# Optimization experiments

Hardware: AMD Instinct MI355X
Metric: run time of the kernel (lower is better)

Reference implementation:

```python
import jax, jax.numpy as jnp
import numpy as np

EPS = 1e-8

def setup_inputs() -> dict:
    key = jax.random.key(0)
    k1, k2, k3, k4, k5 = jax.random.split(key, 5)
    B, S, d, H = 4, 1024, 512, 8
    hd = d // H
    x = jax.random.normal(k1, (B, S, d), dtype=jnp.float32)
    V = jax.random.normal(k2, (B, S, H, hd), dtype=jnp.float32)
    # binary biological mask [B, S, S]
    M = (jax.random.uniform(k3, (B, S, S)) > 0.5).astype(jnp.float32)
    in_proj_w = jax.random.normal(k4, (3 * d, d), dtype=jnp.float32) * 0.02
    in_proj_b = jnp.zeros((3 * d,), dtype=jnp.float32)
    out_w = jax.random.normal(k5, (d, d), dtype=jnp.float32) * 0.02
    out_b = jnp.zeros((d,), dtype=jnp.float32)
    return {"x": x, "V": V, "M": M, "in_proj_w": in_proj_w,
            "in_proj_b": in_proj_b, "out_w": out_w, "out_b": out_b}


def reference(x, V, M, in_proj_w, in_proj_b, out_w, out_b):
    B, S, d = x.shape
    H, hd = V.shape[2], V.shape[3]
    # packed QKV projection (torch MHA in_proj); V slice is computed by torch
    # but its result is discarded, so only Q,K slices influence the output.
    qkv = x @ in_proj_w.T + in_proj_b            # [B, S, 3d]
    q = qkv[..., :d].reshape(B, S, H, hd).transpose(0, 2, 1, 3)        # [B,H,S,hd]
    k = qkv[..., d:2 * d].reshape(B, S, H, hd).transpose(0, 2, 1, 3)   # [B,H,S,hd]
    scores = jnp.einsum("bhqd,bhkd->bhqk", q, k) / jnp.sqrt(jnp.float32(hd))
    A = jax.nn.softmax(scores, axis=-1)           # [B,H,S,S] per-head attn weights
    # biological mask + L1 renormalization (post-hoc, as in original)
    A_sparse = A * M[:, None, :, :]
    norm = jnp.sum(jnp.abs(A_sparse), axis=-1, keepdims=True) + EPS
    A_bar = A_sparse / norm
    # custom V: [B,S,H,hd] -> [B,H,S,hd]
    Vp = V.transpose(0, 2, 1, 3)
    out = jnp.einsum("bhqk,bhkd->bhqd", A_bar, Vp)  # [B,H,S,hd]
    out = out.transpose(0, 2, 1, 3).reshape(B, S, d)
    return out @ out_w.T + out_b
```

## Files before the change

### kernel.cpp

```cpp
#include <hip/hip_runtime.h>
#include <hip/hip_bf16.h>

#define BB 4
#define SS 1024
#define DD 512
#define HH 8
#define HD 64

typedef __attribute__((ext_vector_type(8))) short bf16x8;
typedef __attribute__((ext_vector_type(4))) float f32x4;

static __device__ __forceinline__ unsigned short f2b(float f) {
  union { float f; unsigned int u; } c; c.f = f;
  return (unsigned short)((c.u + 0x7fffu + ((c.u >> 16) & 1u)) >> 16);
}

__global__ __launch_bounds__(256) void prep(
    const float* __restrict__ x, const float* __restrict__ W1,
    const float* __restrict__ Wo, const float* __restrict__ Mmask,
    const float* __restrict__ V, unsigned short* __restrict__ xb,
    unsigned short* __restrict__ W1b, unsigned short* __restrict__ Wob,
    unsigned char* __restrict__ Mpack, unsigned short* __restrict__ Vt) {
  __shared__ float Ls[64][65];
  const int bid = blockIdx.x;
  const int tid = threadIdx.x;

  if (bid < 1408) {
    const float* src; unsigned short* dst; size_t off;
    if (bid < 1024) { src = x;  dst = xb;  off = ((size_t)bid * 256 + tid) * 8; }
    else if (bid < 1280) { src = W1; dst = W1b; off = ((size_t)(bid - 1024) * 256 + tid) * 8; }
    else { src = Wo; dst = Wob; off = ((size_t)(bid - 1280) * 256 + tid) * 8; }
    const float4 a = *(const float4*)(src + off);
    const float4 b = *(const float4*)(src + off + 4);
    union { unsigned short s[8]; uint4 v; } o;
    o.s[0] = f2b(a.x); o.s[1] = f2b(a.y); o.s[2] = f2b(a.z); o.s[3] = f2b(a.w);
    o.s[4] = f2b(b.x); o.s[5] = f2b(b.y); o.s[6] = f2b(b.z); o.s[7] = f2b(b.w);
    *(uint4*)(dst + off) = o.v;
  } else if (bid < 3456) {
    const size_t g = (size_t)(bid - 1408) * 256 + tid;
    const float4 a = *(const float4*)(Mmask + g * 8);
    const float4 b = *(const float4*)(Mmask + g * 8 + 4);
    unsigned v = 0;
    v |= (a.x > 0.5f) ? 1u : 0u;   v |= (a.y > 0.5f) ? 2u : 0u;
    v |= (a.z > 0.5f) ? 4u : 0u;   v |= (a.w > 0.5f) ? 8u : 0u;
    v |= (b.x > 0.5f) ? 16u : 0u;  v |= (b.y > 0.5f) ? 32u : 0u;
    v |= (b.z > 0.5f) ? 64u : 0u;  v |= (b.w > 0.5f) ? 128u : 0u;
    Mpack[g] = (unsigned char)v;
  } else {
    const int id = bid - 3456;
    const int s0 = (id & 15) * 64, h = (id >> 4) & 7, b = id >> 7;
    {
      const int r = tid >> 2, cs = (tid & 3) * 16;
      const float* src = V + ((size_t)((b * SS + s0 + r) * HH) + h) * HD + cs;
#pragma unroll
      for (int j = 0; j < 4; j++) {
        const float4 v = *(const float4*)(src + j * 4);
        Ls[r][cs + j * 4 + 0] = v.x; Ls[r][cs + j * 4 + 1] = v.y;
        Ls[r][cs + j * 4 + 2] = v.z; Ls[r][cs + j * 4 + 3] = v.w;
      }
    }
    __syncthreads();
    {
      const int d = tid >> 2, ss = (tid & 3) * 16;
      union { unsigned short s[16]; uint4 v[2]; } o;
#pragma unroll
      for (int j = 0; j < 16; j++) o.s[j] = f2b(Ls[ss + j][d]);
      unsigned short* dst =
          Vt + ((size_t)((b * HH + h) * HD + d)) * SS + s0 + ss;
      *(uint4*)dst = o.v[0];
      *(uint4*)(dst + 8) = o.v[1];
    }
  }
}

__global__ __launch_bounds__(256) void gemm_qk(
    const unsigned short* __restrict__ xb, const unsigned short* __restrict__ W1b,
    const float* __restrict__ bias, unsigned short* __restrict__ qkb) {
  __shared__ unsigned short As[128][40];
  __shared__ unsigned short Bs[64][40];
  const int tid = threadIdx.x;
  const int lane = tid & 63, wave = tid >> 6;
  const int l16 = lane & 15, quad = lane >> 4;
  const int row0 = blockIdx.y * 128, col0 = blockIdx.x * 64;

  f32x4 acc[2][4];
#pragma unroll
  for (int i = 0; i < 2; i++)
#pragma unroll
    for (int j = 0; j < 4; j++) acc[i][j] = (f32x4){0.f, 0.f, 0.f, 0.f};

  const int ra = tid >> 1, csa = (tid & 1) * 16;
  const int rb = tid >> 2, csb = (tid & 3) * 8;
  const unsigned short* ap = xb + (size_t)(row0 + ra) * DD + csa;
  const unsigned short* bp = W1b + (size_t)(col0 + rb) * DD + csb;

  uint4 pa0 = *(const uint4*)ap, pa1 = *(const uint4*)(ap + 8);
  uint4 pb = *(const uint4*)bp;

  for (int k0 = 0; k0 < DD; k0 += 32) {
    __syncthreads();
    *(uint4*)&As[ra][csa] = pa0;
    *(uint4*)&As[ra][csa + 8] = pa1;
    *(uint4*)&Bs[rb][csb] = pb;
    __syncthreads();
    if (k0 + 32 < DD) {
      pa0 = *(const uint4*)(ap + k0 + 32);
      pa1 = *(const uint4*)(ap + k0 + 40);
      pb = *(const uint4*)(bp + k0 + 32);
    }

    const bf16x8 a0 = *(const bf16x8*)&As[wave * 32 + l16][quad * 8];
    const bf16x8 a1 = *(const bf16x8*)&As[wave * 32 + 16 + l16][quad * 8];
#pragma unroll
    for (int nt = 0; nt < 4; nt++) {
      const bf16x8 bb = *(const bf16x8*)&Bs[nt * 16 + l16][quad * 8];
      acc[0][nt] = __builtin_amdgcn_mfma_f32_16x16x32_bf16(a0, bb, acc[0][nt], 0, 0, 0);
      acc[1][nt] = __builtin_amdgcn_mfma_f32_16x16x32_bf16(a1, bb, acc[1][nt], 0, 0, 0);
    }
  }

#pragma unroll
  for (int nt = 0; nt < 4; nt++) {
    const int col = col0 + nt * 16 + l16;
    const float bv = bias[col];
    const float scale = (col < DD) ? 0.125f : 1.0f;
#pragma unroll
    for (int mi = 0; mi < 2; mi++)
#pragma unroll
      for (int reg = 0; reg < 4; reg++) {
        const int row = row0 + wave * 32 + mi * 16 + quad * 4 + reg;
        qkb[(size_t)row * 1024 + col] = f2b((acc[mi][nt][reg] + bv) * scale);
      }
  }
}

__global__ __launch_bounds__(256) void gemm_out(
    const unsigned short* __restrict__ Ab, const unsigned short* __restrict__ Wob,
    const float* __restrict__ bias, float* __restrict__ out) {
  __shared__ unsigned short As[64][40];
  __shared__ unsigned short Bs[64][40];
  const int tid = threadIdx.x;
  const int lane = tid & 63, wave = tid >> 6;
  const int l16 = lane & 15, quad = lane >> 4;
  const int row0 = blockIdx.y * 64, col0 = blockIdx.x * 64;

  f32x4 acc[4];
#pragma unroll
  for (int j = 0; j < 4; j++) acc[j] = (f32x4){0.f, 0.f, 0.f, 0.f};

  const int r = tid >> 2, cs = (tid & 3) * 8;
  const unsigned short* ap = Ab + (size_t)(row0 + r) * DD + cs;
  const unsigned short* bp = Wob + (size_t)(col0 + r) * DD + cs;

  uint4 pa = *(const uint4*)ap;
  uint4 pb = *(const uint4*)bp;

  for (int k0 = 0; k0 < DD; k0 += 32) {
    __syncthreads();
    *(uint4*)&As[r][cs] = pa;
    *(uint4*)&Bs[r][cs] = pb;
    __syncthreads();
    if (k0 + 32 < DD) {
      pa = *(const uint4*)(ap + k0 + 32);
      pb = *(const uint4*)(bp + k0 + 32);
    }

    const bf16x8 a0 = *(const bf16x8*)&As[wave * 16 + l16][quad * 8];
#pragma unroll
    for (int nt = 0; nt < 4; nt++) {
      const bf16x8 bb = *(const bf16x8*)&Bs[nt * 16 + l16][quad * 8];
      acc[nt] = __builtin_amdgcn_mfma_f32_16x16x32_bf16(a0, bb, acc[nt], 0, 0, 0);
    }
  }

#pragma unroll
  for (int nt = 0; nt < 4; nt++) {
    const int col = col0 + nt * 16 + l16;
    const float bv = bias[col];
#pragma unroll
    for (int reg = 0; reg < 4; reg++) {
      const int row = row0 + wave * 16 + quad * 4 + reg;
      out[(size_t)row * DD + col] = acc[nt][reg] + bv;
    }
  }
}

__global__ __launch_bounds__(256) void flash_attn(
    const unsigned short* __restrict__ qkb, const unsigned short* __restrict__ Vt,
    const unsigned char* __restrict__ Mpack, unsigned short* __restrict__ attnb) {
  __shared__ unsigned short QP[64][72];
  __shared__ unsigned short Ks[64][72];
  __shared__ unsigned short Vs[64][72];
  __shared__ float SmT[4][16];

  const int tid = threadIdx.x;
  const int lane = tid & 63, wave = tid >> 6;
  const int l16 = lane & 15, quad = lane >> 4;
  const int q0 = blockIdx.x * 64;
  const int h = blockIdx.y;
  const int b = blockIdx.z;

  const int r = tid >> 2, cs = (tid & 3) * 16;

  {
    const unsigned short* s = qkb + (size_t)(b * SS + q0 + r) * 1024 + h * HD + cs;
    *(uint4*)&QP[r][cs] = *(const uint4*)s;
    *(uint4*)&QP[r][cs + 8] = *(const uint4*)(s + 8);
  }
  __syncthreads();
  const bf16x8 bQ0 = *(const bf16x8*)&QP[wave * 16 + l16][quad * 8];
  const bf16x8 bQ1 = *(const bf16x8*)&QP[wave * 16 + l16][32 + quad * 8];
  unsigned short(*Ps)[72] = (unsigned short(*)[72]) & QP[wave * 16][0];

  const unsigned char* mrowp =
      Mpack + (size_t)(b * SS + q0 + wave * 16 + l16) * 128;

  float Smp = 0.f;
  f32x4 O[4];
#pragma unroll
  for (int i = 0; i < 4; i++) O[i] = (f32x4){0.f, 0.f, 0.f, 0.f};

  const unsigned short* kp = qkb + (size_t)(b * SS + r) * 1024 + DD + h * HD + cs;
  const unsigned short* vp = Vt + ((size_t)((b * HH + h) * HD + r)) * SS + cs;

  uint4 pk0 = *(const uint4*)kp, pk1 = *(const uint4*)(kp + 8);
  uint4 pv0 = *(const uint4*)vp, pv1 = *(const uint4*)(vp + 8);
  uint2 pm = *(const uint2*)mrowp;

#pragma unroll 4
  for (int i = 0; i < 16; i++) {
    const unsigned mlo = pm.x, mhi = pm.y;

    __syncthreads();
    *(uint4*)&Ks[r][cs] = pk0;
    *(uint4*)&Ks[r][cs + 8] = pk1;
    *(uint4*)&Vs[r][cs] = pv0;
    *(uint4*)&Vs[r][cs + 8] = pv1;
    __syncthreads();

    if (i < 15) {
      const unsigned short* nk = kp + (size_t)(i + 1) * 64 * 1024;
      const unsigned short* nv = vp + (i + 1) * 64;
      pk0 = *(const uint4*)nk; pk1 = *(const uint4*)(nk + 8);
      pv0 = *(const uint4*)nv; pv1 = *(const uint4*)(nv + 8);
      pm = *(const uint2*)(mrowp + (i + 1) * 8);
    }

#pragma unroll
    for (int t = 0; t < 4; t++) {
      const bf16x8 aK0 = *(const bf16x8*)&Ks[t * 16 + l16][quad * 8];
      const bf16x8 aK1 = *(const bf16x8*)&Ks[t * 16 + l16][32 + quad * 8];
      f32x4 a = (f32x4){0.f, 0.f, 0.f, 0.f};
      a = __builtin_amdgcn_mfma_f32_16x16x32_bf16(aK0, bQ0, a, 0, 0, 0);
      a = __builtin_amdgcn_mfma_f32_16x16x32_bf16(aK1, bQ1, a, 0, 0, 0);
      const unsigned nib =
          ((t < 2 ? mlo : mhi) >> ((t & 1) * 16 + quad * 4)) & 0xFu;
      float e0 = __expf(a[0]); e0 = (nib & 1u) ? e0 : 0.f;
      float e1 = __expf(a[1]); e1 = (nib & 2u) ? e1 : 0.f;
      float e2 = __expf(a[2]); e2 = (nib & 4u) ? e2 : 0.f;
      float e3 = __expf(a[3]); e3 = (nib & 8u) ? e3 : 0.f;
      Smp += (e0 + e1) + (e2 + e3);
      uint2 w;
      w.x = (unsigned)f2b(e0) | ((unsigned)f2b(e1) << 16);
      w.y = (unsigned)f2b(e2) | ((unsigned)f2b(e3) << 16);
      *(uint2*)&Ps[l16][t * 16 + quad * 4] = w;
    }

    const bf16x8 aP0 = *(const bf16x8*)&Ps[l16][quad * 8];
    const bf16x8 aP1 = *(const bf16x8*)&Ps[l16][32 + quad * 8];
#pragma unroll
    for (int dt = 0; dt < 4; dt++) {
      const bf16x8 bV0 = *(const bf16x8*)&Vs[dt * 16 + l16][quad * 8];
      const bf16x8 bV1 = *(const bf16x8*)&Vs[dt * 16 + l16][32 + quad * 8];
      O[dt] = __builtin_amdgcn_mfma_f32_16x16x32_bf16(aP0, bV0, O[dt], 0, 0, 0);
      O[dt] = __builtin_amdgcn_mfma_f32_16x16x32_bf16(aP1, bV1, O[dt], 0, 0, 0);
    }
  }

  Smp += __shfl_xor(Smp, 16);
  Smp += __shfl_xor(Smp, 32);
  if (lane < 16) SmT[wave][lane] = Smp;
  float invr[4];
#pragma unroll
  for (int reg = 0; reg < 4; reg++)
    invr[reg] = 1.0f / (SmT[wave][quad * 4 + reg] + 1e-12f);
#pragma unroll
  for (int reg = 0; reg < 4; reg++) {
    const size_t row = (size_t)(b * SS + q0 + wave * 16 + quad * 4 + reg);
#pragma unroll
    for (int dt = 0; dt < 4; dt++)
      attnb[row * DD + h * HD + dt * 16 + l16] = f2b(O[dt][reg] * invr[reg]);
  }
}

extern "C" void kernel_launch(void* const* d_in, const int* in_sizes, int n_in,
                              void* d_out, int out_size, void* d_ws,
                              size_t ws_size, hipStream_t stream) {
  const float* x = (const float*)d_in[0];
  const float* V = (const float*)d_in[1];
  const float* Mmask = (const float*)d_in[2];
  const float* in_proj_w = (const float*)d_in[3];
  const float* in_proj_b = (const float*)d_in[4];
  const float* out_w = (const float*)d_in[5];
  const float* out_b = (const float*)d_in[6];
  float* out = (float*)d_out;

  unsigned char* ws = (unsigned char*)d_ws;
  unsigned short* qkb   = (unsigned short*)(ws);
  unsigned short* xb    = (unsigned short*)(ws + (8ull << 20));
  unsigned short* W1b   = (unsigned short*)(ws + (12ull << 20));
  unsigned short* Wob   = (unsigned short*)(ws + (13ull << 20));
  unsigned short* Vt    = (unsigned short*)(ws + (14ull << 20));
  unsigned short* attnb = (unsigned short*)(ws + (18ull << 20));
  unsigned char*  Mpack = ws + (22ull << 20);

  prep<<<3968, 256, 0, stream>>>(x, in_proj_w, out_w, Mmask, V,
                                 xb, W1b, Wob, Mpack, Vt);
  gemm_qk<<<dim3(16, 32), 256, 0, stream>>>(xb, W1b, in_proj_b, qkb);
  flash_attn<<<dim3(SS / 64, HH, BB), 256, 0, stream>>>(qkb, Vt, Mpack, attnb);
  gemm_out<<<dim3(8, 64), 256, 0, stream>>>(attnb, Wob, out_b, out);
}
```

Measured before the change: 137.0 us.

## Fuse bf16 conversion into QK GEMM and merge it with mask/V prep launch

The separate fp32-to-bf16 conversion of x, W1 and Wo is removed. The QK projection GEMM now loads fp32 directly and converts while staging into shared memory, and gemm_out does the same for Wo. The QK GEMM blocks are folded into the prep kernel alongside mask packing and the V transpose, sharing LDS through a union, so one launch and the bf16 round-trip through global memory are gone. In exchange the GEMMs read twice as many bytes per tile, redo the conversion for each tile that reuses the data, and the mixed-role kernel may hurt scheduling balance.

New measurement: 142.0 us. +3.7%, slower.

```diff
diff --git a/kernel.cpp b/kernel.cpp
--- a/kernel.cpp
+++ b/kernel.cpp
@@ -15,29 +15,88 @@
   return (unsigned short)((c.u + 0x7fffu + ((c.u >> 16) & 1u)) >> 16);
 }
 
-__global__ __launch_bounds__(256) void prep(
+__global__ __launch_bounds__(256) void qk_prep(
     const float* __restrict__ x, const float* __restrict__ W1,
-    const float* __restrict__ Wo, const float* __restrict__ Mmask,
-    const float* __restrict__ V, unsigned short* __restrict__ xb,
-    unsigned short* __restrict__ W1b, unsigned short* __restrict__ Wob,
+    const float* __restrict__ b1, const float* __restrict__ Mmask,
+    const float* __restrict__ V, unsigned short* __restrict__ qkb,
     unsigned char* __restrict__ Mpack, unsigned short* __restrict__ Vt) {
-  __shared__ float Ls[64][65];
-  const int bid = blockIdx.x;
+  union ShU {
+    struct { unsigned short As[128][40]; unsigned short Bs[64][40]; } g;
+    float Ls[64][65];
+  };
+  __shared__ ShU sh;
+  const int u = blockIdx.x;
   const int tid = threadIdx.x;
 
-  if (bid < 1408) {
-    const float* src; unsigned short* dst; size_t off;
-    if (bid < 1024) { src = x;  dst = xb;  off = ((size_t)bid * 256 + tid) * 8; }
-    else if (bid < 1280) { src = W1; dst = W1b; off = ((size_t)(bid - 1024) * 256 + tid) * 8; }
-    else { src = Wo; dst = Wob; off = ((size_t)(bid - 1280) * 256 + tid) * 8; }
-    const float4 a = *(const float4*)(src + off);
-    const float4 b = *(const float4*)(src + off + 4);
-    union { unsigned short s[8]; uint4 v; } o;
-    o.s[0] = f2b(a.x); o.s[1] = f2b(a.y); o.s[2] = f2b(a.z); o.s[3] = f2b(a.w);
-    o.s[4] = f2b(b.x); o.s[5] = f2b(b.y); o.s[6] = f2b(b.z); o.s[7] = f2b(b.w);
-    *(uint4*)(dst + off) = o.v;
-  } else if (bid < 3456) {
-    const size_t g = (size_t)(bid - 1408) * 256 + tid;
+  if (u < 512) {
+    const int lane = tid & 63, wave = tid >> 6;
+    const int l16 = lane & 15, quad = lane >> 4;
+    const int row0 = (u >> 4) * 128, col0 = (u & 15) * 64;
+
+    f32x4 acc[2][4];
+#pragma unroll
+    for (int i = 0; i < 2; i++)
+#pragma unroll
+      for (int j = 0; j < 4; j++) acc[i][j] = (f32x4){0.f, 0.f, 0.f, 0.f};
+
+    const int ra = tid >> 1, csa = (tid & 1) * 16;
+    const int rb = tid >> 2, csb = (tid & 3) * 8;
+    const float* ap = x + (size_t)(row0 + ra) * DD + csa;
+    const float* bp = W1 + (size_t)(col0 + rb) * DD + csb;
+
+    float4 pa0 = *(const float4*)ap, pa1 = *(const float4*)(ap + 4);
+    float4 pa2 = *(const float4*)(ap + 8), pa3 = *(const float4*)(ap + 12);
+    float4 pb0 = *(const float4*)bp, pb1 = *(const float4*)(bp + 4);
+
+    for (int k0 = 0; k0 < DD; k0 += 32) {
+      __syncthreads();
+      {
+        union { unsigned short s[16]; uint4 v[2]; } o;
+        o.s[0] = f2b(pa0.x); o.s[1] = f2b(pa0.y); o.s[2] = f2b(pa0.z); o.s[3] = f2b(pa0.w);
+        o.s[4] = f2b(pa1.x); o.s[5] = f2b(pa1.y); o.s[6] = f2b(pa1.z); o.s[7] = f2b(pa1.w);
+        o.s[8] = f2b(pa2.x); o.s[9] = f2b(pa2.y); o.s[10] = f2b(pa2.z); o.s[11] = f2b(pa2.w);
+        o.s[12] = f2b(pa3.x); o.s[13] = f2b(pa3.y); o.s[14] = f2b(pa3.z); o.s[15] = f2b(pa3.w);
+        *(uint4*)&sh.g.As[ra][csa] = o.v[0];
+        *(uint4*)&sh.g.As[ra][csa + 8] = o.v[1];
+      }
+      {
+        union { unsigned short s[8]; uint4 v; } o;
+        o.s[0] = f2b(pb0.x); o.s[1] = f2b(pb0.y); o.s[2] = f2b(pb0.z); o.s[3] = f2b(pb0.w);
+        o.s[4] = f2b(pb1.x); o.s[5] = f2b(pb1.y); o.s[6] = f2b(pb1.z); o.s[7] = f2b(pb1.w);
+        *(uint4*)&sh.g.Bs[rb][csb] = o.v;
+      }
+      __syncthreads();
+      if (k0 + 32 < DD) {
+        pa0 = *(const float4*)(ap + k0 + 32); pa1 = *(const float4*)(ap + k0 + 36);
+        pa2 = *(const float4*)(ap + k0 + 40); pa3 = *(const float4*)(ap + k0 + 44);
+        pb0 = *(const float4*)(bp + k0 + 32); pb1 = *(const float4*)(bp + k0 + 36);
+      }
+
+      const bf16x8 a0 = *(const bf16x8*)&sh.g.As[wave * 32 + l16][quad * 8];
+      const bf16x8 a1 = *(const bf16x8*)&sh.g.As[wave * 32 + 16 + l16][quad * 8];
+#pragma unroll
+      for (int nt = 0; nt < 4; nt++) {
+        const bf16x8 bb = *(const bf16x8*)&sh.g.Bs[nt * 16 + l16][quad * 8];
+        acc[0][nt] = __builtin_amdgcn_mfma_f32_16x16x32_bf16(a0, bb, acc[0][nt], 0, 0, 0);
+        acc[1][nt] = __builtin_amdgcn_mfma_f32_16x16x32_bf16(a1, bb, acc[1][nt], 0, 0, 0);
+      }
+    }
+
+#pragma unroll
+    for (int nt = 0; nt < 4; nt++) {
+      const int col = col0 + nt * 16 + l16;
+      const float bv = b1[col];
+      const float scale = (col < DD) ? 0.125f : 1.0f;
+#pragma unroll
+      for (int mi = 0; mi < 2; mi++)
+#pragma unroll
+        for (int reg = 0; reg < 4; reg++) {
+          const int row = row0 + wave * 32 + mi * 16 + quad * 4 + reg;
+          qkb[(size_t)row * 1024 + col] = f2b((acc[mi][nt][reg] + bv) * scale);
+        }
+    }
+  } else if (u < 2560) {
+    const size_t g = (size_t)(u - 512) * 256 + tid;
     const float4 a = *(const float4*)(Mmask + g * 8);
     const float4 b = *(const float4*)(Mmask + g * 8 + 4);
     unsigned v = 0;
@@ -47,7 +106,7 @@
     v |= (b.z > 0.5f) ? 64u : 0u;  v |= (b.w > 0.5f) ? 128u : 0u;
     Mpack[g] = (unsigned char)v;
   } else {
-    const int id = bid - 3456;
+    const int id = u - 2560;
     const int s0 = (id & 15) * 64, h = (id >> 4) & 7, b = id >> 7;
     {
       const int r = tid >> 2, cs = (tid & 3) * 16;
@@ -55,8 +114,8 @@
 #pragma unroll
       for (int j = 0; j < 4; j++) {
         const float4 v = *(const float4*)(src + j * 4);
-        Ls[r][cs + j * 4 + 0] = v.x; Ls[r][cs + j * 4 + 1] = v.y;
-        Ls[r][cs + j * 4 + 2] = v.z; Ls[r][cs + j * 4 + 3] = v.w;
+        sh.Ls[r][cs + j * 4 + 0] = v.x; sh.Ls[r][cs + j * 4 + 1] = v.y;
+        sh.Ls[r][cs + j * 4 + 2] = v.z; sh.Ls[r][cs + j * 4 + 3] = v.w;
       }
     }
     __syncthreads();
@@ -64,123 +123,11 @@
       const int d = tid >> 2, ss = (tid & 3) * 16;
       union { unsigned short s[16]; uint4 v[2]; } o;
 #pragma unroll
-      for (int j = 0; j < 16; j++) o.s[j] = f2b(Ls[ss + j][d]);
+      for (int j = 0; j < 16; j++) o.s[j] = f2b(sh.Ls[ss + j][d]);
       unsigned short* dst =
           Vt + ((size_t)((b * HH + h) * HD + d)) * SS + s0 + ss;
       *(uint4*)dst = o.v[0];
       *(uint4*)(dst + 8) = o.v[1];
-    }
-  }
-}
-
-__global__ __launch_bounds__(256) void gemm_qk(
-    const unsigned short* __restrict__ xb, const unsigned short* __restrict__ W1b,
-    const float* __restrict__ bias, unsigned short* __restrict__ qkb) {
-  __shared__ unsigned short As[128][40];
-  __shared__ unsigned short Bs[64][40];
-  const int tid = threadIdx.x;
-  const int lane = tid & 63, wave = tid >> 6;
-  const int l16 = lane & 15, quad = lane >> 4;
-  const int row0 = blockIdx.y * 128, col0 = blockIdx.x * 64;
-
-  f32x4 acc[2][4];
-#pragma unroll
-  for (int i = 0; i < 2; i++)
-#pragma unroll
-    for (int j = 0; j < 4; j++) acc[i][j] = (f32x4){0.f, 0.f, 0.f, 0.f};
-
-  const int ra = tid >> 1, csa = (tid & 1) * 16;
-  const int rb = tid >> 2, csb = (tid & 3) * 8;
-  const unsigned short* ap = xb + (size_t)(row0 + ra) * DD + csa;
-  const unsigned short* bp = W1b + (size_t)(col0 + rb) * DD + csb;
-
-  uint4 pa0 = *(const uint4*)ap, pa1 = *(const uint4*)(ap + 8);
-  uint4 pb = *(const uint4*)bp;
-
-  for (int k0 = 0; k0 < DD; k0 += 32) {
-    __syncthreads();
-    *(uint4*)&As[ra][csa] = pa0;
-    *(uint4*)&As[ra][csa + 8] = pa1;
-    *(uint4*)&Bs[rb][csb] = pb;
-    __syncthreads();
-    if (k0 + 32 < DD) {
-      pa0 = *(const uint4*)(ap + k0 + 32);
-      pa1 = *(const uint4*)(ap + k0 + 40);
-      pb = *(const uint4*)(bp + k0 + 32);
-    }
-
-    const bf16x8 a0 = *(const bf16x8*)&As[wave * 32 + l16][quad * 8];
-    const bf16x8 a1 = *(const bf16x8*)&As[wave * 32 + 16 + l16][quad * 8];
-#pragma unroll
-    for (int nt = 0; nt < 4; nt++) {
-      const bf16x8 bb = *(const bf16x8*)&Bs[nt * 16 + l16][quad * 8];
-      acc[0][nt] = __builtin_amdgcn_mfma_f32_16x16x32_bf16(a0, bb, acc[0][nt], 0, 0, 0);
-      acc[1][nt] = __builtin_amdgcn_mfma_f32_16x16x32_bf16(a1, bb, acc[1][nt], 0, 0, 0);
-    }
-  }
-
-#pragma unroll
-  for (int nt = 0; nt < 4; nt++) {
-    const int col = col0 + nt * 16 + l16;
-    const float bv = bias[col];
-    const float scale = (col < DD) ? 0.125f : 1.0f;
-#pragma unroll
-    for (int mi = 0; mi < 2; mi++)
-#pragma unroll
-      for (int reg = 0; reg < 4; reg++) {
-        const int row = row0 + wave * 32 + mi * 16 + quad * 4 + reg;
-        qkb[(size_t)row * 1024 + col] = f2b((acc[mi][nt][reg] + bv) * scale);
-      }
-  }
-}
-
-__global__ __launch_bounds__(256) void gemm_out(
-    const unsigned short* __restrict__ Ab, const unsigned short* __restrict__ Wob,
-    const float* __restrict__ bias, float* __restrict__ out) {
-  __shared__ unsigned short As[64][40];
-  __shared__ unsigned short Bs[64][40];
-  const int tid = threadIdx.x;
-  const int lane = tid & 63, wave = tid >> 6;
-  const int l16 = lane & 15, quad = lane >> 4;
-  const int row0 = blockIdx.y * 64, col0 = blockIdx.x * 64;
-
-  f32x4 acc[4];
-#pragma unroll
-  for (int j = 0; j < 4; j++) acc[j] = (f32x4){0.f, 0.f, 0.f, 0.f};
-
-  const int r = tid >> 2, cs = (tid & 3) * 8;
-  const unsigned short* ap = Ab + (size_t)(row0 + r) * DD + cs;
-  const unsigned short* bp = Wob + (size_t)(col0 + r) * DD + cs;
-
-  uint4 pa = *(const uint4*)ap;
-  uint4 pb = *(const uint4*)bp;
-
-  for (int k0 = 0; k0 < DD; k0 += 32) {
-    __syncthreads();
-    *(uint4*)&As[r][cs] = pa;
-    *(uint4*)&Bs[r][cs] = pb;
-    __syncthreads();
-    if (k0 + 32 < DD) {
-      pa = *(const uint4*)(ap + k0 + 32);
-      pb = *(const uint4*)(bp + k0 + 32);
-    }
-
-    const bf16x8 a0 = *(const bf16x8*)&As[wave * 16 + l16][quad * 8];
-#pragma unroll
-    for (int nt = 0; nt < 4; nt++) {
-      const bf16x8 bb = *(const bf16x8*)&Bs[nt * 16 + l16][quad * 8];
-      acc[nt] = __builtin_amdgcn_mfma_f32_16x16x32_bf16(a0, bb, acc[nt], 0, 0, 0);
-    }
-  }
-
-#pragma unroll
-  for (int nt = 0; nt < 4; nt++) {
-    const int col = col0 + nt * 16 + l16;
-    const float bv = bias[col];
-#pragma unroll
-    for (int reg = 0; reg < 4; reg++) {
-      const int row = row0 + wave * 16 + quad * 4 + reg;
-      out[(size_t)row * DD + col] = acc[nt][reg] + bv;
     }
   }
 }
@@ -293,6 +240,63 @@
   }
 }
 
+__global__ __launch_bounds__(256) void gemm_out(
+    const unsigned short* __restrict__ Ab, const float* __restrict__ Wo,
+    const float* __restrict__ bias, float* __restrict__ out) {
+  __shared__ unsigned short As[64][40];
+  __shared__ unsigned short Bs[64][40];
+  const int tid = threadIdx.x;
+  const int lane = tid & 63, wave = tid >> 6;
+  const int l16 = lane & 15, quad = lane >> 4;
+  const int row0 = blockIdx.y * 64, col0 = blockIdx.x * 64;
+
+  f32x4 acc[4];
+#pragma unroll
+  for (int j = 0; j < 4; j++) acc[j] = (f32x4){0.f, 0.f, 0.f, 0.f};
+
+  const int r = tid >> 2, cs = (tid & 3) * 8;
+  const unsigned short* ap = Ab + (size_t)(row0 + r) * DD + cs;
+  const float* bp = Wo + (size_t)(col0 + r) * DD + cs;
+
+  uint4 pa = *(const uint4*)ap;
+  float4 pb0 = *(const float4*)bp, pb1 = *(const float4*)(bp + 4);
+
+  for (int k0 = 0; k0 < DD; k0 += 32) {
+    __syncthreads();
+    *(uint4*)&As[r][cs] = pa;
+    {
+      union { unsigned short s[8]; uint4 v; } o;
+      o.s[0] = f2b(pb0.x); o.s[1] = f2b(pb0.y); o.s[2] = f2b(pb0.z); o.s[3] = f2b(pb0.w);
+      o.s[4] = f2b(pb1.x); o.s[5] = f2b(pb1.y); o.s[6] = f2b(pb1.z); o.s[7] = f2b(pb1.w);
+      *(uint4*)&Bs[r][cs] = o.v;
+    }
+    __syncthreads();
+    if (k0 + 32 < DD) {
+      pa = *(const uint4*)(ap + k0 + 32);
+      pb0 = *(const float4*)(bp + k0 + 32);
+      pb1 = *(const float4*)(bp + k0 + 36);
+    }
+
+    const bf16x8 a0 = *(const bf16x8*)&As[wave * 16 + l16][quad * 8];
+#pragma unroll
+    for (int nt = 0; nt < 4; nt++) {
+      const bf16x8 bb = *(const bf16x8*)&Bs[nt * 16 + l16][quad * 8];
+      acc[nt] = __builtin_amdgcn_mfma_f32_16x16x32_bf16(a0, bb, acc[nt], 0, 0, 0);
+    }
+  }
+
+#pragma unroll
+  for (int nt = 0; nt < 4; nt++) {
+    const int col = col0 + nt * 16 + l16;
+    const float bv = bias[col];
+#pragma unroll
+    for (int reg = 0; reg < 4; reg++) {
+      const int row = row0 + wave * 16 + quad * 4 + reg;
+      out[(size_t)row * DD + col] = acc[nt][reg] + bv;
+    }
+  }
+}
+
 extern "C" void kernel_launch(void* const* d_in, const int* in_sizes, int n_in,
                               void* d_out, int out_size, void* d_ws,
                               size_t ws_size, hipStream_t stream) {
@@ -307,16 +311,12 @@
 
   unsigned char* ws = (unsigned char*)d_ws;
   unsigned short* qkb   = (unsigned short*)(ws);
-  unsigned short* xb    = (unsigned short*)(ws + (8ull << 20));
-  unsigned short* W1b   = (unsigned short*)(ws + (12ull << 20));
-  unsigned short* Wob   = (unsigned short*)(ws + (13ull << 20));
-  unsigned short* Vt    = (unsigned short*)(ws + (14ull << 20));
-  unsigned short* attnb = (unsigned short*)(ws + (18ull << 20));
-  unsigned char*  Mpack = ws + (22ull << 20);
-
-  prep<<<3968, 256, 0, stream>>>(x, in_proj_w, out_w, Mmask, V,
-                                 xb, W1b, Wob, Mpack, Vt);
-  gemm_qk<<<dim3(16, 32), 256, 0, stream>>>(xb, W1b, in_proj_b, qkb);
+  unsigned short* Vt    = (unsigned short*)(ws + (8ull << 20));
+  unsigned short* attnb = (unsigned short*)(ws + (12ull << 20));
+  unsigned char*  Mpack = ws + (16ull << 20);
+
+  qk_prep<<<3072, 256, 0, stream>>>(x, in_proj_w, in_proj_b, Mmask, V,
+                                    qkb, Mpack, Vt);
   flash_attn<<<dim3(SS / 64, HH, BB), 256, 0, stream>>>(qkb, Vt, Mpack, attnb);
-  gemm_out<<<dim3(8, 64), 256, 0, stream>>>(attnb, Wob, out_b, out);
-}
+  gemm_out<<<dim3(8, 64), 256, 0, stream>>>(attnb, out_w, out_b, out);
+}
```
